# Optimization experiments

Hardware: AMD Instinct MI355X
Metric: run time of the kernel (lower is better)

Reference implementation:

```python
import jax, jax.numpy as jnp
import numpy as np

B, D, H = 4096, 2048, 2048

def setup_inputs() -> dict:
    key = jax.random.key(0)
    ks = jax.random.split(key, 16)
    s = 0.02  # small scale to keep tanh/sigmoid out of saturation
    inp = {
        'input_': jax.random.normal(ks[0], (B, D), jnp.float32),
        'h_prev': jax.random.normal(ks[1], (B, H), jnp.float32),
        'c_prev': jax.random.normal(ks[2], (B, H), jnp.float32),
        'w_xi': jax.random.normal(ks[3], (D, H), jnp.float32) * s,
        'w_hi': jax.random.normal(ks[4], (H, H), jnp.float32) * s,
        'w_ci': jax.random.normal(ks[5], (H, H), jnp.float32) * s,
        'w_xf': jax.random.normal(ks[6], (D, H), jnp.float32) * s,
        'w_hf': jax.random.normal(ks[7], (H, H), jnp.float32) * s,
        'w_cf': jax.random.normal(ks[8], (H, H), jnp.float32) * s,
        'w_xg': jax.random.normal(ks[9], (D, H), jnp.float32) * s,
        'w_hg': jax.random.normal(ks[10], (H, H), jnp.float32) * s,
        'w_xo': jax.random.normal(ks[11], (D, H), jnp.float32) * s,
        'w_ho': jax.random.normal(ks[12], (H, H), jnp.float32) * s,
        'w_co': jax.random.normal(ks[13], (H, H), jnp.float32) * s,
        'w_c':  jax.random.normal(ks[14], (H, H), jnp.float32) * s,
        'w_i':  jax.random.normal(ks[15], (D, H), jnp.float32) * s,
        'b_i': jnp.zeros((H,), jnp.float32),
        'b_f': jnp.zeros((H,), jnp.float32),
        'b_g': jnp.zeros((H,), jnp.float32),
        'b_o': jnp.zeros((H,), jnp.float32),
    }
    return inp

def reference(input_, h_prev, c_prev,
              w_xi, w_hi, w_ci, w_xf, w_hf, w_cf, w_xg, w_hg,
              w_xo, w_ho, w_co, w_c, w_i,
              b_i, b_f, b_g, b_o):
    # Fuse the x- and h-path GEMMs into concatenated matmuls (math-identical).
    wx = jnp.concatenate([w_xi, w_xf, w_xg, w_xo, w_i], axis=1)   # [D, 5H]
    wh = jnp.concatenate([w_hi, w_hf, w_hg, w_ho], axis=1)        # [H, 4H]
    wc = jnp.concatenate([w_ci, w_cf], axis=1)                    # [H, 2H]
    xz = input_ @ wx                                              # [B, 5H]
    hz = h_prev @ wh                                              # [B, 4H]
    cz = c_prev @ wc                                              # [B, 2H]
    Hd = w_hi.shape[0]
    i = xz[:, 0*Hd:1*Hd] + hz[:, 0*Hd:1*Hd] + cz[:, 0*Hd:1*Hd] + b_i
    f = xz[:, 1*Hd:2*Hd] + hz[:, 1*Hd:2*Hd] + cz[:, 1*Hd:2*Hd] + b_f
    g = xz[:, 2*Hd:3*Hd] + hz[:, 2*Hd:3*Hd] + b_g
    c = jax.nn.sigmoid(f) * c_prev + jax.nn.sigmoid(i) * jnp.tanh(g)
    o = xz[:, 3*Hd:4*Hd] + hz[:, 3*Hd:4*Hd] + c @ w_co + b_o
    h = jnp.tanh(o) * (jnp.tanh(c) @ w_c + xz[:, 4*Hd:5*Hd])
    return (h, c)
```

## Files before the change

### kernel.cpp

```cpp
#include <hip/hip_runtime.h>
#include <cstdint>
#include <cstddef>

typedef unsigned short u16;
typedef __bf16 bf16x8 __attribute__((ext_vector_type(8)));
typedef float f32x4 __attribute__((ext_vector_type(4)));
typedef u16 u16x8 __attribute__((ext_vector_type(8)));

#define B_DIM 4096
#define H_DIM 2048
#define BH 8388608

__device__ __forceinline__ float b2f(u16 x) {
  union { uint32_t u; float f; } v;
  v.u = ((uint32_t)x) << 16;
  return v.f;
}
__device__ __forceinline__ u16 f2b(float f) {
  union { float f; uint32_t u; } v;
  v.f = f;
  uint32_t r = v.u + 0x7FFFu + ((v.u >> 16) & 1u);
  return (u16)(r >> 16);
}
__device__ __forceinline__ float sigm(float x) { return 1.0f / (1.0f + __expf(-x)); }

typedef __attribute__((address_space(1))) void gv_t;
typedef __attribute__((address_space(3))) void lv_t;
__device__ __forceinline__ void g2lds16(const void* g, void* l) {
  __builtin_amdgcn_global_load_lds((gv_t*)g, (lv_t*)l, 16, 0, 0);
}

#define MFMA_BF16 __builtin_amdgcn_mfma_f32_16x16x32_bf16

struct CvtParams { const float* src[3]; u16* dst[3]; };

__global__ __launch_bounds__(256) void cvt_k(CvtParams p) {
  const float* __restrict__ s = p.src[blockIdx.y];
  u16* __restrict__ d = p.dst[blockIdx.y];
  size_t idx = ((size_t)blockIdx.x * 256 + threadIdx.x) * 8;
  float4 a = *(const float4*)(s + idx);
  float4 b = *(const float4*)(s + idx + 4);
  u16x8 o;
  o[0] = f2b(a.x); o[1] = f2b(a.y); o[2] = f2b(a.z); o[3] = f2b(a.w);
  o[4] = f2b(b.x); o[5] = f2b(b.y); o[6] = f2b(b.z); o[7] = f2b(b.w);
  *(u16x8*)(d + idx) = o;
}

struct TransParams {
  const float* src[13];
  u16* dst[13];
  int dstride[13];
};

__global__ __launch_bounds__(256) void transpose_k(TransParams p) {
  __shared__ u16 lds[64][72];
  const int mat = blockIdx.z;
  const float* __restrict__ src = p.src[mat];
  u16* __restrict__ dst = p.dst[mat];
  const int dstride = p.dstride[mat];
  const int tk = blockIdx.y * 64;
  const int tn = blockIdx.x * 64;
  const int t = threadIdx.x;
  const int lr = t >> 3;
  const int lc = (t & 7) * 8;
#pragma unroll
  for (int half = 0; half < 2; half++) {
    int r = lr + half * 32;
    const float4* g = (const float4*)(src + (size_t)(tk + r) * 2048 + tn + lc);
    float4 a = g[0], b = g[1];
    u16x8 t8;
    t8[0] = f2b(a.x); t8[1] = f2b(a.y); t8[2] = f2b(a.z); t8[3] = f2b(a.w);
    t8[4] = f2b(b.x); t8[5] = f2b(b.y); t8[6] = f2b(b.z); t8[7] = f2b(b.w);
    *(u16x8*)&lds[r][lc] = t8;
  }
  __syncthreads();
#pragma unroll
  for (int half = 0; half < 2; half++) {
    int n = lr + half * 32;
    u16x8 tmp;
#pragma unroll
    for (int j = 0; j < 8; j++) tmp[j] = lds[lc + j][n];
    *(u16x8*)(dst + (size_t)(tn + n) * dstride + tk + lc) = tmp;
  }
}

__device__ __forceinline__ void kloop256(
    const u16* __restrict__ A0, const u16* __restrict__ A1, const u16* __restrict__ A2,
    const u16* __restrict__ Wt, const int NT, const long Ktot,
    const int m0, const int n0,
    u16* lA0, u16* lA1, u16* lB0, u16* lB1,
    f32x4 (&acc)[8][4]) {
  const int tid = threadIdx.x;
  const int wave = tid >> 6, lane = tid & 63;
  const int fm = lane & 15, fkc = lane >> 4;
  const int x7 = fm & 7;
  const int wm = (wave >> 2) * 128, wn = (wave & 3) * 64;
  const int lr = tid >> 3;
  const int chunk = (tid & 7) ^ (lr & 7);
  const int stageOff = wave * 512;

  int raOff[8], rbOff[4];
#pragma unroll
  for (int i = 0; i < 8; i++) raOff[i] = (wm + i * 16 + fm) * 64;
#pragma unroll
  for (int j = 0; j < 4; j++) rbOff[j] = (wn + j * 16 + fm) * 64;
  const int so0 = ((fkc ^ x7) << 3);
  const int so1 = (((4 + fkc) ^ x7) << 3);

  auto stA = [&](int tt, int a, u16* dst) {
    const int seg = tt >> 5;
    const u16* base = (seg == 0) ? A0 : ((seg == 1) ? A1 : A2);
    const u16* src = base + (size_t)(m0 + a * 64 + lr) * 2048 + ((tt & 31) << 6) + (chunk << 3);
    g2lds16(src, dst + a * 4096 + stageOff);
  };
  auto stB = [&](int tt, int b, u16* dst) {
    const u16* src = Wt + (size_t)(n0 + b * 64 + lr) * Ktot + ((size_t)tt << 6) + (chunk << 3);
    g2lds16(src, dst + b * 4096 + stageOff);
  };

#pragma unroll
  for (int a = 0; a < 4; a++) stA(0, a, lA0);
#pragma unroll
  for (int b = 0; b < 4; b++) stB(0, b, lB0);
  const int t1p = (1 < NT) ? 1 : 0;
#pragma unroll
  for (int a = 0; a < 4; a++) stA(t1p, a, lA1);
  asm volatile("s_waitcnt vmcnt(4)" ::: "memory");
  __builtin_amdgcn_sched_barrier(0);
  __builtin_amdgcn_s_barrier();
  __builtin_amdgcn_sched_barrier(0);

  for (int t = 0; t < NT; ++t) {
    u16* lAp = (t & 1) ? lA1 : lA0;
    u16* lBp = (t & 1) ? lB1 : lB0;
    u16* lBq = (t & 1) ? lB0 : lB1;
    const int tn1 = (t + 1 < NT) ? t + 1 : NT - 1;
    const int tn2 = (t + 2 < NT) ? t + 2 : NT - 1;

    bf16x8 a0[8], b0[4];
#pragma unroll
    for (int i = 0; i < 8; i++) a0[i] = *(const bf16x8*)&lAp[raOff[i] + so0];
#pragma unroll
    for (int j = 0; j < 4; j++) b0[j] = *(const bf16x8*)&lBp[rbOff[j] + so0];
    stB(tn1, 0, lBq);
    stB(tn1, 1, lBq);
    __builtin_amdgcn_s_barrier();
    asm volatile("s_waitcnt lgkmcnt(0)" ::: "memory");
    __builtin_amdgcn_sched_barrier(0);
    __builtin_amdgcn_s_setprio(1);
#pragma unroll
    for (int i = 0; i < 8; i++) {
      acc[i][0] = MFMA_BF16(a0[i], b0[0], acc[i][0], 0, 0, 0);
      acc[i][1] = MFMA_BF16(a0[i], b0[1], acc[i][1], 0, 0, 0);
    }
    __builtin_amdgcn_s_setprio(0);
    __builtin_amdgcn_sched_barrier(0);
    __builtin_amdgcn_s_barrier();
    __builtin_amdgcn_sched_barrier(0);

    stB(tn1, 2, lBq);
    stB(tn1, 3, lBq);
    __builtin_amdgcn_s_barrier();
    __builtin_amdgcn_sched_barrier(0);
    __builtin_amdgcn_s_setprio(1);
#pragma unroll
    for (int i = 0; i < 8; i++) {
      acc[i][2] = MFMA_BF16(a0[i], b0[2], acc[i][2], 0, 0, 0);
      acc[i][3] = MFMA_BF16(a0[i], b0[3], acc[i][3], 0, 0, 0);
    }
    __builtin_amdgcn_s_setprio(0);
    __builtin_amdgcn_sched_barrier(0);
    __builtin_amdgcn_s_barrier();
    __builtin_amdgcn_sched_barrier(0);

    bf16x8 a1[8], b1[4];
#pragma unroll
    for (int i = 0; i < 8; i++) a1[i] = *(const bf16x8*)&lAp[raOff[i] + so1];
#pragma unroll
    for (int j = 0; j < 4; j++) b1[j] = *(const bf16x8*)&lBp[rbOff[j] + so1];
    __builtin_amdgcn_s_barrier();
    asm volatile("s_waitcnt lgkmcnt(0)" ::: "memory");
    __builtin_amdgcn_sched_barrier(0);
    __builtin_amdgcn_s_setprio(1);
#pragma unroll
    for (int i = 0; i < 8; i++) {
      acc[i][0] = MFMA_BF16(a1[i], b1[0], acc[i][0], 0, 0, 0);
      acc[i][1] = MFMA_BF16(a1[i], b1[1], acc[i][1], 0, 0, 0);
    }
    __builtin_amdgcn_s_setprio(0);
    __builtin_amdgcn_sched_barrier(0);
    __builtin_amdgcn_s_barrier();
    __builtin_amdgcn_sched_barrier(0);

    stA(tn2, 0, lAp);
    stA(tn2, 1, lAp);
    stA(tn2, 2, lAp);
    stA(tn2, 3, lAp);
    __builtin_amdgcn_s_barrier();
    __builtin_amdgcn_sched_barrier(0);
    __builtin_amdgcn_s_setprio(1);
#pragma unroll
    for (int i = 0; i < 8; i++) {
      acc[i][2] = MFMA_BF16(a1[i], b1[2], acc[i][2], 0, 0, 0);
      acc[i][3] = MFMA_BF16(a1[i], b1[3], acc[i][3], 0, 0, 0);
    }
    __builtin_amdgcn_s_setprio(0);
    asm volatile("s_waitcnt vmcnt(4)" ::: "memory");
    __builtin_amdgcn_sched_barrier(0);
    __builtin_amdgcn_s_barrier();
    __builtin_amdgcn_sched_barrier(0);
  }
}

struct Gemm256Desc {
  const u16* A0; const u16* A1; const u16* A2;
  const u16* Wt; u16* C; int nseg;
};
struct Gemm256Params { Gemm256Desc d[5]; };

__global__ __launch_bounds__(512) void gemm256_multi(Gemm256Params p) {
  const Gemm256Desc d = p.d[blockIdx.z];
  __shared__ u16 lA[2][16384];
  __shared__ u16 lB[2][16384];
  const int bid = blockIdx.y * 8 + blockIdx.x;
  const int swz = (bid & 7) * 16 + (bid >> 3);
  const int m0 = (swz >> 3) * 256, n0 = (swz & 7) * 256;
  const int NT = d.nseg << 5;
  const long Ktot = (long)NT << 6;

  f32x4 acc[8][4];
#pragma unroll
  for (int i = 0; i < 8; i++)
#pragma unroll
    for (int j = 0; j < 4; j++) acc[i][j] = (f32x4)0.0f;

  kloop256(d.A0, d.A1, d.A2, d.Wt, NT, Ktot, m0, n0, lA[0], lA[1], lB[0], lB[1], acc);

  const int lane = threadIdx.x & 63, wave = threadIdx.x >> 6;
  const int fm = lane & 15, quad = lane >> 4;
  const int wm = (wave >> 2) * 128, wn = (wave & 3) * 64;
#pragma unroll
  for (int i = 0; i < 8; i++)
#pragma unroll
    for (int j = 0; j < 4; j++)
#pragma unroll
      for (int r = 0; r < 4; r++) {
        size_t row = (size_t)(m0 + wm + i * 16 + quad * 4 + r);
        size_t col = (size_t)(n0 + wn + j * 16 + fm);
        d.C[row * 2048 + col] = f2b(acc[i][j][r]);
      }
}

struct GemmResParams {
  const u16* A[2]; const u16* W[2];
  u16* t1; float* t2;
};

__global__ __launch_bounds__(512) void gemm256_res(GemmResParams p) {
  const int z = blockIdx.z;
  __shared__ u16 lA[2][16384];
  __shared__ u16 lB[2][16384];
  const int bid = blockIdx.y * 8 + blockIdx.x;
  const int swz = (bid & 7) * 16 + (bid >> 3);
  const int m0 = (swz >> 3) * 256, n0 = (swz & 7) * 256;

  f32x4 acc[8][4];
#pragma unroll
  for (int i = 0; i < 8; i++)
#pragma unroll
    for (int j = 0; j < 4; j++) acc[i][j] = (f32x4)0.0f;

  kloop256(p.A[z], nullptr, nullptr, p.W[z], 32, 2048, m0, n0, lA[0], lA[1], lB[0], lB[1], acc);

  const int lane = threadIdx.x & 63, wave = threadIdx.x >> 6;
  const int fm = lane & 15, quad = lane >> 4;
  const int wm = (wave >> 2) * 128, wn = (wave & 3) * 64;
  if (z == 0) {
#pragma unroll
    for (int i = 0; i < 8; i++)
#pragma unroll
      for (int j = 0; j < 4; j++)
#pragma unroll
        for (int r = 0; r < 4; r++) {
          size_t row = (size_t)(m0 + wm + i * 16 + quad * 4 + r);
          size_t col = (size_t)(n0 + wn + j * 16 + fm);
          p.t1[row * 2048 + col] = f2b(acc[i][j][r]);
        }
  } else {
#pragma unroll
    for (int i = 0; i < 8; i++)
#pragma unroll
      for (int j = 0; j < 4; j++)
#pragma unroll
        for (int r = 0; r < 4; r++) {
          size_t row = (size_t)(m0 + wm + i * 16 + quad * 4 + r);
          size_t col = (size_t)(n0 + wn + j * 16 + fm);
          p.t2[row * 2048 + col] = acc[i][j][r];
        }
  }
}

__global__ __launch_bounds__(256) void ew1_k(
    u16* __restrict__ zi, const u16* __restrict__ zf, u16* __restrict__ zg,
    const float* __restrict__ cprev, const float* __restrict__ bi,
    const float* __restrict__ bff, const float* __restrict__ bg,
    float* __restrict__ c_out) {
  size_t idx = ((size_t)blockIdx.x * 256 + threadIdx.x) * 8;
  int col = (int)(idx & (H_DIM - 1));
  u16x8 vzi = *(const u16x8*)(zi + idx);
  u16x8 vzf = *(const u16x8*)(zf + idx);
  u16x8 vzg = *(const u16x8*)(zg + idx);
  float4 cp0 = *(const float4*)(cprev + idx);
  float4 cp1 = *(const float4*)(cprev + idx + 4);
  float4 bi0 = *(const float4*)(bi + col), bi1 = *(const float4*)(bi + col + 4);
  float4 bf0 = *(const float4*)(bff + col), bf1 = *(const float4*)(bff + col + 4);
  float4 bg0 = *(const float4*)(bg + col), bg1 = *(const float4*)(bg + col + 4);
  float cpv[8] = {cp0.x, cp0.y, cp0.z, cp0.w, cp1.x, cp1.y, cp1.z, cp1.w};
  float biv[8] = {bi0.x, bi0.y, bi0.z, bi0.w, bi1.x, bi1.y, bi1.z, bi1.w};
  float bfv[8] = {bf0.x, bf0.y, bf0.z, bf0.w, bf1.x, bf1.y, bf1.z, bf1.w};
  float bgv[8] = {bg0.x, bg0.y, bg0.z, bg0.w, bg1.x, bg1.y, bg1.z, bg1.w};
  float cv[8], tcv[8];
#pragma unroll
  for (int e = 0; e < 8; e++) {
    float iv = b2f(vzi[e]) + biv[e];
    float fv = b2f(vzf[e]) + bfv[e];
    float gv = b2f(vzg[e]) + bgv[e];
    float c = sigm(fv) * cpv[e] + sigm(iv) * tanhf(gv);
    cv[e] = c;
    tcv[e] = tanhf(c);
  }
  u16x8 cb8, tc8;
#pragma unroll
  for (int e = 0; e < 8; e++) { cb8[e] = f2b(cv[e]); tc8[e] = f2b(tcv[e]); }
  *(u16x8*)(zi + idx) = cb8;
  *(u16x8*)(zg + idx) = tc8;
  float4 c0 = {cv[0], cv[1], cv[2], cv[3]}, c1 = {cv[4], cv[5], cv[6], cv[7]};
  *(float4*)(c_out + idx) = c0;
  *(float4*)(c_out + idx + 4) = c1;
}

__global__ __launch_bounds__(256) void ew2_k(
    const u16* __restrict__ zo, const u16* __restrict__ zr,
    const u16* __restrict__ t1, const float* __restrict__ t2,
    const float* __restrict__ bo, float* __restrict__ h) {
  size_t idx = ((size_t)blockIdx.x * 256 + threadIdx.x) * 8;
  int col = (int)(idx & (H_DIM - 1));
  u16x8 vo = *(const u16x8*)(zo + idx);
  u16x8 vr = *(const u16x8*)(zr + idx);
  u16x8 v1 = *(const u16x8*)(t1 + idx);
  float4 t2a = *(const float4*)(t2 + idx);
  float4 t2b = *(const float4*)(t2 + idx + 4);
  float4 bo0 = *(const float4*)(bo + col);
  float4 bo1 = *(const float4*)(bo + col + 4);
  float t2v[8] = {t2a.x, t2a.y, t2a.z, t2a.w, t2b.x, t2b.y, t2b.z, t2b.w};
  float bov[8] = {bo0.x, bo0.y, bo0.z, bo0.w, bo1.x, bo1.y, bo1.z, bo1.w};
  float hv[8];
#pragma unroll
  for (int e = 0; e < 8; e++) {
    float ov = b2f(vo[e]) + b2f(v1[e]) + bov[e];
    hv[e] = tanhf(ov) * (b2f(vr[e]) + t2v[e]);
  }
  float4 h0 = {hv[0], hv[1], hv[2], hv[3]}, h1 = {hv[4], hv[5], hv[6], hv[7]};
  *(float4*)(h + idx) = h0;
  *(float4*)(h + idx + 4) = h1;
}

extern "C" void kernel_launch(void* const* d_in, const int* in_sizes, int n_in,
                              void* d_out, int out_size, void* d_ws, size_t ws_size,
                              hipStream_t stream) {
  const float* input_ = (const float*)d_in[0];
  const float* h_prev = (const float*)d_in[1];
  const float* c_prev = (const float*)d_in[2];
  const float* w_xi = (const float*)d_in[3];
  const float* w_hi = (const float*)d_in[4];
  const float* w_ci = (const float*)d_in[5];
  const float* w_xf = (const float*)d_in[6];
  const float* w_hf = (const float*)d_in[7];
  const float* w_cf = (const float*)d_in[8];
  const float* w_xg = (const float*)d_in[9];
  const float* w_hg = (const float*)d_in[10];
  const float* w_xo = (const float*)d_in[11];
  const float* w_ho = (const float*)d_in[12];
  const float* w_co = (const float*)d_in[13];
  const float* w_c  = (const float*)d_in[14];
  const float* w_i  = (const float*)d_in[15];
  const float* b_i  = (const float*)d_in[16];
  const float* b_f  = (const float*)d_in[17];
  const float* b_g  = (const float*)d_in[18];
  const float* b_o  = (const float*)d_in[19];

  u16* ws = (u16*)d_ws;
  u16* WtI  = ws;
  u16* WtF  = WtI  + (size_t)2048 * 6144;
  u16* WtG  = WtF  + (size_t)2048 * 6144;
  u16* WtO  = WtG  + (size_t)2048 * 4096;
  u16* WtR  = WtO  + (size_t)2048 * 4096;
  u16* WtCO = WtR  + (size_t)2048 * 2048;
  u16* WtC  = WtCO + (size_t)2048 * 2048;
  u16* zi   = WtC  + (size_t)2048 * 2048;
  u16* zf   = zi + (size_t)BH;
  u16* zg   = zf + (size_t)BH;
  u16* zo   = zg + (size_t)BH;
  u16* zr   = zo + (size_t)BH;

  u16* t1buf = WtG;
  float* t2buf = (float*)WtI;

  u16* ob16 = (u16*)d_out;
  u16* xb = ob16;
  u16* hb = ob16 + (size_t)BH;
  u16* cb = ob16 + (size_t)2 * BH;
  float* out_f = (float*)d_out;
  float* h_out = out_f;
  float* c_out = out_f + (size_t)BH;

  CvtParams cp;
  cp.src[0] = input_; cp.src[1] = h_prev; cp.src[2] = c_prev;
  cp.dst[0] = xb; cp.dst[1] = hb; cp.dst[2] = cb;
  cvt_k<<<dim3(BH / 2048, 3), 256, 0, stream>>>(cp);

  TransParams tp;
  const float* srcs[13] = {w_xi, w_hi, w_ci, w_xf, w_hf, w_cf, w_xg, w_hg, w_xo, w_ho, w_i, w_co, w_c};
  u16* dsts[13] = {WtI, WtI + 2048, WtI + 4096, WtF, WtF + 2048, WtF + 4096,
                   WtG, WtG + 2048, WtO, WtO + 2048, WtR, WtCO, WtC};
  int strides[13] = {6144, 6144, 6144, 6144, 6144, 6144, 4096, 4096, 4096, 4096, 2048, 2048, 2048};
  for (int i = 0; i < 13; i++) { tp.src[i] = srcs[i]; tp.dst[i] = dsts[i]; tp.dstride[i] = strides[i]; }
  transpose_k<<<dim3(32, 32, 13), 256, 0, stream>>>(tp);

  Gemm256Params g1;
  g1.d[0] = {xb, hb, cb, WtI, zi, 3};
  g1.d[1] = {xb, hb, cb, WtF, zf, 3};
  g1.d[2] = {xb, hb, nullptr, WtG, zg, 2};
  g1.d[3] = {xb, hb, nullptr, WtO, zo, 2};
  g1.d[4] = {xb, nullptr, nullptr, WtR, zr, 1};
  gemm256_multi<<<dim3(8, 16, 5), 512, 0, stream>>>(g1);

  ew1_k<<<dim3(BH / 2048), 256, 0, stream>>>(zi, zf, zg, c_prev, b_i, b_f, b_g, c_out);

  GemmResParams gr;
  gr.A[0] = zi; gr.A[1] = zg; gr.W[0] = WtCO; gr.W[1] = WtC;
  gr.t1 = t1buf; gr.t2 = t2buf;
  gemm256_res<<<dim3(8, 16, 2), 512, 0, stream>>>(gr);

  ew2_k<<<dim3(BH / 2048), 256, 0, stream>>>(zo, zr, t1buf, t2buf, b_o, h_out);
}
```

Measured before the change: 804.5 us.

## Restructure GEMM k-loop into quadrant MFMA phases with fewer barriers

Rewrites the inner k-loop of the 256x256 bf16 GEMM. Each iteration now loads both k-halves of the A and B fragments up front and issues the MFMAs in four quadrant groups. It drops several block barriers and sched_barriers, and moves the vmcnt wait between the two A-stage halves. Both GEMM kernels also get launch_bounds(512, 2) to request two blocks per CU. With 128 KB of LDS per block a second block likely cannot fit, and the tighter register budget could force spills of the 128-register accumulator.

```diff
diff --git a/kernel.cpp b/kernel.cpp
--- a/kernel.cpp
+++ b/kernel.cpp
@@ -122,13 +122,12 @@
   for (int a = 0; a < 4; a++) stA(0, a, lA0);
 #pragma unroll
   for (int b = 0; b < 4; b++) stB(0, b, lB0);
-  const int t1p = (1 < NT) ? 1 : 0;
-#pragma unroll
-  for (int a = 0; a < 4; a++) stA(t1p, a, lA1);
+  const int t1c = (1 < NT) ? 1 : 0;
+#pragma unroll
+  for (int a = 0; a < 4; a++) stA(t1c, a, lA1);
   asm volatile("s_waitcnt vmcnt(4)" ::: "memory");
-  __builtin_amdgcn_sched_barrier(0);
   __builtin_amdgcn_s_barrier();
-  __builtin_amdgcn_sched_barrier(0);
+  asm volatile("" ::: "memory");
 
   for (int t = 0; t < NT; ++t) {
     u16* lAp = (t & 1) ? lA1 : lA0;
@@ -137,79 +136,85 @@
     const int tn1 = (t + 1 < NT) ? t + 1 : NT - 1;
     const int tn2 = (t + 2 < NT) ? t + 2 : NT - 1;
 
-    bf16x8 a0[8], b0[4];
-#pragma unroll
-    for (int i = 0; i < 8; i++) a0[i] = *(const bf16x8*)&lAp[raOff[i] + so0];
-#pragma unroll
-    for (int j = 0; j < 4; j++) b0[j] = *(const bf16x8*)&lBp[rbOff[j] + so0];
     stB(tn1, 0, lBq);
     stB(tn1, 1, lBq);
-    __builtin_amdgcn_s_barrier();
-    asm volatile("s_waitcnt lgkmcnt(0)" ::: "memory");
-    __builtin_amdgcn_sched_barrier(0);
-    __builtin_amdgcn_s_setprio(1);
-#pragma unroll
-    for (int i = 0; i < 8; i++) {
-      acc[i][0] = MFMA_BF16(a0[i], b0[0], acc[i][0], 0, 0, 0);
-      acc[i][1] = MFMA_BF16(a0[i], b0[1], acc[i][1], 0, 0, 0);
-    }
-    __builtin_amdgcn_s_setprio(0);
-    __builtin_amdgcn_sched_barrier(0);
-    __builtin_amdgcn_s_barrier();
-    __builtin_amdgcn_sched_barrier(0);
-
     stB(tn1, 2, lBq);
     stB(tn1, 3, lBq);
+    bf16x8 b01[2][2], a03[4][2], a47[4][2];
+#pragma unroll
+    for (int j = 0; j < 2; j++) {
+      b01[j][0] = *(const bf16x8*)&lBp[rbOff[j] + so0];
+      b01[j][1] = *(const bf16x8*)&lBp[rbOff[j] + so1];
+    }
+#pragma unroll
+    for (int i = 0; i < 4; i++) {
+      a03[i][0] = *(const bf16x8*)&lAp[raOff[i] + so0];
+      a03[i][1] = *(const bf16x8*)&lAp[raOff[i] + so1];
+    }
+#pragma unroll
+    for (int i = 0; i < 4; i++) {
+      a47[i][0] = *(const bf16x8*)&lAp[raOff[4 + i] + so0];
+      a47[i][1] = *(const bf16x8*)&lAp[raOff[4 + i] + so1];
+    }
+    __builtin_amdgcn_s_setprio(1);
+#pragma unroll
+    for (int ks = 0; ks < 2; ks++)
+#pragma unroll
+      for (int i = 0; i < 4; i++) {
+        acc[i][0] = MFMA_BF16(a03[i][ks], b01[0][ks], acc[i][0], 0, 0, 0);
+        acc[i][1] = MFMA_BF16(a03[i][ks], b01[1][ks], acc[i][1], 0, 0, 0);
+      }
+    __builtin_amdgcn_s_setprio(0);
+
+    bf16x8 b23[2][2];
+#pragma unroll
+    for (int j = 0; j < 2; j++) {
+      b23[j][0] = *(const bf16x8*)&lBp[rbOff[2 + j] + so0];
+      b23[j][1] = *(const bf16x8*)&lBp[rbOff[2 + j] + so1];
+    }
+    __builtin_amdgcn_s_setprio(1);
+#pragma unroll
+    for (int ks = 0; ks < 2; ks++)
+#pragma unroll
+      for (int i = 0; i < 4; i++) {
+        acc[4 + i][0] = MFMA_BF16(a47[i][ks], b01[0][ks], acc[4 + i][0], 0, 0, 0);
+        acc[4 + i][1] = MFMA_BF16(a47[i][ks], b01[1][ks], acc[4 + i][1], 0, 0, 0);
+      }
+    __builtin_amdgcn_s_setprio(0);
+
     __builtin_amdgcn_s_barrier();
-    __builtin_amdgcn_sched_barrier(0);
-    __builtin_amdgcn_s_setprio(1);
-#pragma unroll
-    for (int i = 0; i < 8; i++) {
-      acc[i][2] = MFMA_BF16(a0[i], b0[2], acc[i][2], 0, 0, 0);
-      acc[i][3] = MFMA_BF16(a0[i], b0[3], acc[i][3], 0, 0, 0);
-    }
-    __builtin_amdgcn_s_setprio(0);
-    __builtin_amdgcn_sched_barrier(0);
-    __builtin_amdgcn_s_barrier();
-    __builtin_amdgcn_sched_barrier(0);
-
-    bf16x8 a1[8], b1[4];
-#pragma unroll
-    for (int i = 0; i < 8; i++) a1[i] = *(const bf16x8*)&lAp[raOff[i] + so1];
-#pragma unroll
-    for (int j = 0; j < 4; j++) b1[j] = *(const bf16x8*)&lBp[rbOff[j] + so1];
-    __builtin_amdgcn_s_barrier();
-    asm volatile("s_waitcnt lgkmcnt(0)" ::: "memory");
-    __builtin_amdgcn_sched_barrier(0);
-    __builtin_amdgcn_s_setprio(1);
-#pragma unroll
-    for (int i = 0; i < 8; i++) {
-      acc[i][0] = MFMA_BF16(a1[i], b1[0], acc[i][0], 0, 0, 0);
-      acc[i][1] = MFMA_BF16(a1[i], b1[1], acc[i][1], 0, 0, 0);
-    }
-    __builtin_amdgcn_s_setprio(0);
-    __builtin_amdgcn_sched_barrier(0);
-    __builtin_amdgcn_s_barrier();
-    __builtin_amdgcn_sched_barrier(0);
+    asm volatile("" ::: "memory");
 
     stA(tn2, 0, lAp);
     stA(tn2, 1, lAp);
+    __builtin_amdgcn_s_setprio(1);
+#pragma unroll
+    for (int ks = 0; ks < 2; ks++)
+#pragma unroll
+      for (int i = 0; i < 4; i++) {
+        acc[i][2] = MFMA_BF16(a03[i][ks], b23[0][ks], acc[i][2], 0, 0, 0);
+        acc[i][3] = MFMA_BF16(a03[i][ks], b23[1][ks], acc[i][3], 0, 0, 0);
+      }
+    __builtin_amdgcn_s_setprio(0);
+
+    asm volatile("s_waitcnt vmcnt(2)" ::: "memory");
+    __builtin_amdgcn_s_barrier();
+    asm volatile("" ::: "memory");
+
     stA(tn2, 2, lAp);
     stA(tn2, 3, lAp);
-    __builtin_amdgcn_s_barrier();
-    __builtin_amdgcn_sched_barrier(0);
     __builtin_amdgcn_s_setprio(1);
 #pragma unroll
-    for (int i = 0; i < 8; i++) {
-      acc[i][2] = MFMA_BF16(a1[i], b1[2], acc[i][2], 0, 0, 0);
-      acc[i][3] = MFMA_BF16(a1[i], b1[3], acc[i][3], 0, 0, 0);
-    }
+    for (int ks = 0; ks < 2; ks++)
+#pragma unroll
+      for (int i = 0; i < 4; i++) {
+        acc[4 + i][2] = MFMA_BF16(a47[i][ks], b23[0][ks], acc[4 + i][2], 0, 0, 0);
+        acc[4 + i][3] = MFMA_BF16(a47[i][ks], b23[1][ks], acc[4 + i][3], 0, 0, 0);
+      }
     __builtin_amdgcn_s_setprio(0);
-    asm volatile("s_waitcnt vmcnt(4)" ::: "memory");
-    __builtin_amdgcn_sched_barrier(0);
-    __builtin_amdgcn_s_barrier();
-    __builtin_amdgcn_sched_barrier(0);
-  }
+  }
+
+  asm volatile("s_waitcnt vmcnt(0)" ::: "memory");
 }
 
 struct Gemm256Desc {
@@ -218,7 +223,7 @@
 };
 struct Gemm256Params { Gemm256Desc d[5]; };
 
-__global__ __launch_bounds__(512) void gemm256_multi(Gemm256Params p) {
+__global__ __launch_bounds__(512, 2) void gemm256_multi(Gemm256Params p) {
   const Gemm256Desc d = p.d[blockIdx.z];
   __shared__ u16 lA[2][16384];
   __shared__ u16 lB[2][16384];
@@ -256,7 +261,7 @@
   u16* t1; float* t2;
 };
 
-__global__ __launch_bounds__(512) void gemm256_res(GemmResParams p) {
+__global__ __launch_bounds__(512, 2) void gemm256_res(GemmResParams p) {
   const int z = blockIdx.z;
   __shared__ u16 lA[2][16384];
   __shared__ u16 lB[2][16384];
```

New measurement: 811.1 us. No clear change (+0.8%).
